# Performance work log

Measured on AMD Instinct MI355X. Metric: run time of the kernel, lower is better.

## Reference

```python
import jax, jax.numpy as jnp
import numpy as np

NUM_HEADS = 16
NUM_HIDDENS = 1024
NEG_INF = -1e6


def setup_inputs() -> dict:
    key = jax.random.key(0)
    ks = jax.random.split(key, 8)
    B, S, D = 2, 2048, NUM_HIDDENS
    scale = 1.0 / np.sqrt(D)
    return {
        "q": jax.random.normal(ks[0], (B, S, D), jnp.float32),
        "k": jax.random.normal(ks[1], (B, S, D), jnp.float32),
        "v": jax.random.normal(ks[2], (B, S, D), jnp.float32),
        # nn.Linear weights have shape (out_features, in_features)
        "Wq": jax.random.normal(ks[3], (D, D), jnp.float32) * scale,
        "Wk": jax.random.normal(ks[4], (D, D), jnp.float32) * scale,
        "Wv": jax.random.normal(ks[5], (D, D), jnp.float32) * scale,
        "Wo": jax.random.normal(ks[6], (D, D), jnp.float32) * scale,
        "valid_len": jax.random.randint(ks[7], (B,), 1, 2048 + 1, jnp.int32),
    }


def _unpack_heads(x, nh):
    # (B, S, H) -> (B*nh, S, H//nh), matching Unpack_base_head
    B, S, H = x.shape
    return x.reshape(B, S, nh, H // nh).transpose(0, 2, 1, 3).reshape(B * nh, S, H // nh)


def _merge_heads(x, nh):
    # Faithful to Merge_base_head: (B*nh, S, dh) -> (B, nh, S, dh)
    # -> permute(0,2,3,1) -> (B, S, dh, nh) -> (B, S, dh*nh)
    Bnh, S, dh = x.shape
    B = Bnh // nh
    x = x.reshape(B, nh, S, dh).transpose(0, 2, 3, 1)
    return x.reshape(B, S, dh * nh)


def reference(q, k, v, Wq, Wk, Wv, Wo, valid_len):
    nh = NUM_HEADS
    # projections (bias=False); Linear: x @ W.T
    qh = _unpack_heads(q @ Wq.T, nh)  # (B*nh, S, dh)
    kh = _unpack_heads(k @ Wk.T, nh)
    vh = _unpack_heads(v @ Wv.T, nh)
    dh = qh.shape[-1]
    scores = jnp.einsum("bqd,bkd->bqk", qh, kh) / jnp.sqrt(jnp.float32(dh))
    # repeat_interleave valid_len by num_heads along dim 0
    vl = jnp.repeat(valid_len, nh)  # (B*nh,)
    key_pos = jnp.arange(scores.shape[-1])  # (S,)
    mask = key_pos[None, None, :] < vl[:, None, None]  # (B*nh, 1, S)
    scores = jnp.where(mask, scores, NEG_INF)
    attn = jax.nn.softmax(scores, axis=-1)  # dropout=0.0 (eval) -> identity
    out = jnp.einsum("bqk,bkd->bqd", attn, vh)  # (B*nh, S, dh)
    out = _merge_heads(out, nh) @ Wo.T  # (B, S, H)
    return out, attn
```

## Files before the change

kernel.cpp:

```cpp
#include <hip/hip_runtime.h>
#include <stdint.h>

#define SB 2048
#define DB 1024
#define NHB 16
#define DHB 64

typedef __attribute__((ext_vector_type(8))) short short8;
typedef __attribute__((ext_vector_type(4))) short short4v;
typedef __attribute__((ext_vector_type(4))) float f32x4;

#define SC2 0.18033688011112042f

__device__ __forceinline__ unsigned short f2bf(float f) {
  union { float f; uint32_t u; } v; v.f = f;
  uint32_t u = v.u;
  return (unsigned short)((u + 0x7FFFu + ((u >> 16) & 1u)) >> 16);
}

__device__ __forceinline__ void gld16(const void* g, void* l) {
  __builtin_amdgcn_global_load_lds(
      (const __attribute__((address_space(1))) void*)g,
      (__attribute__((address_space(3))) void*)l, 16, 0, 0);
}

__device__ __forceinline__ int xcd_swz(int bid, int nwg) {
  return (bid & 7) * (nwg >> 3) + (bid >> 3);
}

struct ConvArgs {
  const float* s[6];
  unsigned short* d[6];
  int n[6];
};

__global__ __launch_bounds__(256) void conv_kernel(ConvArgs a) {
  const int t = blockIdx.y;
  const float* __restrict__ src = a.s[t];
  unsigned short* __restrict__ dst = a.d[t];
  const int n8 = a.n[t] >> 3;
  for (int i = blockIdx.x * 256 + threadIdx.x; i < n8; i += gridDim.x * 256) {
    const f32x4* p = (const f32x4*)src + (size_t)i * 2;
    f32x4 x = p[0], y = p[1];
    short8 o;
    o[0] = (short)f2bf(x[0]); o[1] = (short)f2bf(x[1]);
    o[2] = (short)f2bf(x[2]); o[3] = (short)f2bf(x[3]);
    o[4] = (short)f2bf(y[0]); o[5] = (short)f2bf(y[1]);
    o[6] = (short)f2bf(y[2]); o[7] = (short)f2bf(y[3]);
    *(short8*)(dst + (size_t)i * 8) = o;
  }
}

__global__ __launch_bounds__(256) void woperm_kernel(
    const float* __restrict__ Wo, unsigned short* __restrict__ Wob) {
  for (int i = blockIdx.x * 256 + threadIdx.x; i < DB * DB; i += gridDim.x * 256) {
    int o = i >> 10, cp = i & 1023;
    int src = (o << 10) + ((cp & 63) << 4) + (cp >> 6);
    Wob[i] = f2bf(Wo[src]);
  }
}

struct GemmArgs {
  const unsigned short* A[3];
  const unsigned short* B[3];
  void* O[3];
  int mode[3];
};

__global__ __launch_bounds__(256) void gemm128(GemmArgs ga) {
  __shared__ unsigned short SH[17408];
  unsigned short* Ab = SH;
  unsigned short* Bb = SH + 8192;

  const int z = blockIdx.y;
  const unsigned short* __restrict__ A = ga.A[z];
  const unsigned short* __restrict__ Bw = ga.B[z];
  const int mode = ga.mode[z];

  const int tid = threadIdx.x;
  const int w = tid >> 6, lane = tid & 63;
  const int g = lane >> 4, li = lane & 15;
  const int wm = w >> 1, wn = w & 1;
  const int l = xcd_swz(blockIdx.x, 256);
  const int m0 = (l >> 3) * 128, n0 = (l & 7) * 128;

  const int srow = lane >> 3;
  const int sg = (lane & 7) ^ srow;

  f32x4 acc[4][4];
  #pragma unroll
  for (int i = 0; i < 4; ++i)
    #pragma unroll
    for (int j = 0; j < 4; ++j)
      #pragma unroll
      for (int e = 0; e < 4; ++e) acc[i][j][e] = 0.f;

  for (int k0 = 0; k0 < DB; k0 += 64) {
    __syncthreads();
    #pragma unroll
    for (int i = 0; i < 4; ++i) {
      int c = w * 4 + i;
      gld16(A + (size_t)(m0 + c * 8 + srow) * DB + k0 + sg * 8, Ab + c * 512);
      gld16(Bw + (size_t)(n0 + c * 8 + srow) * DB + k0 + sg * 8, Bb + c * 512);
    }
    __syncthreads();
    short8 af[4][2], bf[4][2];
    #pragma unroll
    for (int mf = 0; mf < 4; ++mf)
      #pragma unroll
      for (int ks = 0; ks < 2; ++ks)
        af[mf][ks] = *(const short8*)&Ab[(wm * 64 + mf * 16 + li) * 64 +
                                         (((ks * 4 + g) ^ (li & 7)) << 3)];
    #pragma unroll
    for (int nf = 0; nf < 4; ++nf)
      #pragma unroll
      for (int ks = 0; ks < 2; ++ks)
        bf[nf][ks] = *(const short8*)&Bb[(wn * 64 + nf * 16 + li) * 64 +
                                         (((ks * 4 + g) ^ (li & 7)) << 3)];
    __builtin_amdgcn_s_setprio(1);
    #pragma unroll
    for (int ks = 0; ks < 2; ++ks)
      #pragma unroll
      for (int mf = 0; mf < 4; ++mf)
        #pragma unroll
        for (int nf = 0; nf < 4; ++nf)
          acc[mf][nf] = __builtin_amdgcn_mfma_f32_16x16x32_bf16(
              af[mf][ks], bf[nf][ks], acc[mf][nf], 0, 0, 0);
    __builtin_amdgcn_s_setprio(0);
  }

  if (mode == 0) {
    unsigned short* O = (unsigned short*)ga.O[z];
    #pragma unroll
    for (int mf = 0; mf < 4; ++mf)
      #pragma unroll
      for (int nf = 0; nf < 4; ++nf)
        #pragma unroll
        for (int r = 0; r < 4; ++r) {
          int row = m0 + wm * 64 + mf * 16 + g * 4 + r;
          int col = n0 + wn * 64 + nf * 16 + li;
          int b_ = row >> 11, s_ = row & 2047;
          int h = col >> 6, dp = col & 63;
          O[((size_t)(b_ * NHB + h) * SB + s_) * DHB + dp] = f2bf(acc[mf][nf][r]);
        }
  } else {
    unsigned short* O = (unsigned short*)ga.O[z];
    __syncthreads();
    #pragma unroll
    for (int mf = 0; mf < 4; ++mf)
      #pragma unroll
      for (int nf = 0; nf < 4; ++nf) {
        short4v pk;
        #pragma unroll
        for (int r = 0; r < 4; ++r) pk[r] = (short)f2bf(acc[mf][nf][r]);
        *(short4v*)&SH[(size_t)(wn * 64 + nf * 16 + li) * 136 +
                       wm * 64 + mf * 16 + g * 4] = pk;
      }
    __syncthreads();
    int c = tid >> 1, rh = tid & 1;
    int col = n0 + c;
    int h = col >> 6, dp = col & 63;
    int b_ = m0 >> 11, s0 = (m0 & 2047) + rh * 64;
    unsigned short* dst = O + ((size_t)(b_ * NHB + h) * DHB + dp) * SB + s0;
    #pragma unroll
    for (int j = 0; j < 8; ++j)
      *(short8*)(dst + j * 8) = *(const short8*)&SH[c * 136 + rh * 64 + j * 8];
  }
}

__global__ __launch_bounds__(256) void attn_kernel(
    const unsigned short* __restrict__ Qh, const unsigned short* __restrict__ Kh,
    const unsigned short* __restrict__ Vt, const int* __restrict__ valid_len,
    float* __restrict__ attn_out, unsigned short* __restrict__ Mg)
{
  __shared__ unsigned short Kb[2][4096];
  __shared__ unsigned short Vb[2][4096];
  __shared__ unsigned short P[64][72];

  const int tid = threadIdx.x;
  const int wave = tid >> 6, lane = tid & 63;
  const int g = lane >> 4, li = lane & 15;
  const int lsw = xcd_swz(blockIdx.x, 1024);
  const int xcd = lsw >> 7, j = lsw & 127;
  const int bh = ((j >> 6) << 4) + xcd * 2 + ((j >> 5) & 1);
  const int q0 = (j & 31) * 64;
  const int b_ = bh >> 4;
  const int vl = valid_len[b_];
  const int nkt = min(32, (vl + 63) >> 6);

  const int srow = lane >> 3;
  const int sg = (lane & 7) ^ srow;

  const size_t kbase = (size_t)bh * SB * DHB;
  const size_t vbase = (size_t)bh * DHB * SB;

  const int qrow_l = q0 + wave * 16 + li;
  short8 qa[2];
  qa[0] = *(const short8*)(Qh + ((size_t)bh * SB + qrow_l) * DHB + g * 8);
  qa[1] = *(const short8*)(Qh + ((size_t)bh * SB + qrow_l) * DHB + 32 + g * 8);

  float lQ = 0.f;

  {
    const int c = wave * 2;
    gld16(Kh + kbase + (size_t)(c * 8 + srow) * DHB + sg * 8, &Kb[0][c * 512]);
    gld16(Kh + kbase + (size_t)((c + 1) * 8 + srow) * DHB + sg * 8,
          &Kb[0][(c + 1) * 512]);
    int cur = 0;
    for (int kti = 0; kti < nkt; ++kti) {
      __syncthreads();
      if (kti + 1 < nkt) {
        int kn = (kti + 1) * 64;
        gld16(Kh + kbase + (size_t)(kn + c * 8 + srow) * DHB + sg * 8,
              &Kb[cur ^ 1][c * 512]);
        gld16(Kh + kbase + (size_t)(kn + (c + 1) * 8 + srow) * DHB + sg * 8,
              &Kb[cur ^ 1][(c + 1) * 512]);
      }
      const int kt = kti * 64;
      f32x4 sc[4];
      #pragma unroll
      for (int nf = 0; nf < 4; ++nf)
        #pragma unroll
        for (int e = 0; e < 4; ++e) sc[nf][e] = 0.f;
      __builtin_amdgcn_s_setprio(1);
      #pragma unroll
      for (int ks = 0; ks < 2; ++ks)
        #pragma unroll
        for (int nf = 0; nf < 4; ++nf) {
          short8 kbf = *(const short8*)&Kb[cur][(nf * 16 + li) * 64 +
                                               (((ks * 4 + g) ^ (li & 7)) << 3)];
          sc[nf] = __builtin_amdgcn_mfma_f32_16x16x32_bf16(kbf, qa[ks], sc[nf], 0, 0, 0);
        }
      __builtin_amdgcn_s_setprio(0);
      float la = 0.f;
      #pragma unroll
      for (int nf = 0; nf < 4; ++nf)
        #pragma unroll
        for (int r = 0; r < 4; ++r) {
          int key = kt + nf * 16 + g * 4 + r;
          float s2 = (key < vl) ? sc[nf][r] * SC2 : -1.5e6f;
          la += exp2f(s2);
        }
      lQ += la;
      cur ^= 1;
    }
  }
  __syncthreads();

  float L = lQ;
  L += __shfl_xor(L, 16);
  L += __shfl_xor(L, 32);
  const float rlQ = 1.f / L;

  f32x4 oacc[4];
  #pragma unroll
  for (int nf = 0; nf < 4; ++nf)
    #pragma unroll
    for (int e = 0; e < 4; ++e) oacc[nf][e] = 0.f;

  {
    const int c = wave * 2;
    gld16(Kh + kbase + (size_t)(c * 8 + srow) * DHB + sg * 8, &Kb[0][c * 512]);
    gld16(Kh + kbase + (size_t)((c + 1) * 8 + srow) * DHB + sg * 8,
          &Kb[0][(c + 1) * 512]);
    gld16(Vt + vbase + (size_t)(c * 8 + srow) * SB + sg * 8, &Vb[0][c * 512]);
    gld16(Vt + vbase + (size_t)((c + 1) * 8 + srow) * SB + sg * 8,
          &Vb[0][(c + 1) * 512]);
    int cur = 0;
    for (int kti = 0; kti < nkt; ++kti) {
      __syncthreads();
      if (kti + 1 < nkt) {
        int kn = (kti + 1) * 64;
        gld16(Kh + kbase + (size_t)(kn + c * 8 + srow) * DHB + sg * 8,
              &Kb[cur ^ 1][c * 512]);
        gld16(Kh + kbase + (size_t)(kn + (c + 1) * 8 + srow) * DHB + sg * 8,
              &Kb[cur ^ 1][(c + 1) * 512]);
        gld16(Vt + vbase + (size_t)(c * 8 + srow) * SB + kn + sg * 8,
              &Vb[cur ^ 1][c * 512]);
        gld16(Vt + vbase + (size_t)((c + 1) * 8 + srow) * SB + kn + sg * 8,
              &Vb[cur ^ 1][(c + 1) * 512]);
      }
      const int kt = kti * 64;
      f32x4 sc[4];
      #pragma unroll
      for (int nf = 0; nf < 4; ++nf)
        #pragma unroll
        for (int e = 0; e < 4; ++e) sc[nf][e] = 0.f;
      __builtin_amdgcn_s_setprio(1);
      #pragma unroll
      for (int ks = 0; ks < 2; ++ks)
        #pragma unroll
        for (int nf = 0; nf < 4; ++nf) {
          short8 kbf = *(const short8*)&Kb[cur][(nf * 16 + li) * 64 +
                                               (((ks * 4 + g) ^ (li & 7)) << 3)];
          sc[nf] = __builtin_amdgcn_mfma_f32_16x16x32_bf16(kbf, qa[ks], sc[nf], 0, 0, 0);
        }
      __builtin_amdgcn_s_setprio(0);
      #pragma unroll
      for (int nf = 0; nf < 4; ++nf) {
        short4v pk;
        #pragma unroll
        for (int r = 0; r < 4; ++r) {
          int key = kt + nf * 16 + g * 4 + r;
          float s2 = (key < vl) ? sc[nf][r] * SC2 : -1.5e6f;
          float p = exp2f(s2) * rlQ;
          sc[nf][r] = p;
          pk[r] = (short)f2bf(p);
        }
        __builtin_nontemporal_store(
            sc[nf],
            (f32x4*)(attn_out + (size_t)bh * SB * SB + (size_t)qrow_l * SB +
                     kt + nf * 16 + g * 4));
        *(short4v*)&P[wave * 16 + li][nf * 16 + g * 4] = pk;
      }
      __builtin_amdgcn_s_setprio(1);
      #pragma unroll
      for (int ks = 0; ks < 2; ++ks) {
        short8 pa = *(const short8*)&P[wave * 16 + li][ks * 32 + g * 8];
        #pragma unroll
        for (int nf = 0; nf < 4; ++nf) {
          short8 vbf = *(const short8*)&Vb[cur][(nf * 16 + li) * 64 +
                                               (((ks * 4 + g) ^ (li & 7)) << 3)];
          oacc[nf] = __builtin_amdgcn_mfma_f32_16x16x32_bf16(pa, vbf, oacc[nf], 0, 0, 0);
        }
      }
      __builtin_amdgcn_s_setprio(0);
      cur ^= 1;
    }
  }

  {
    int c0 = nkt * 64;
    int rem4 = (SB - c0) >> 2;
    if (rem4 > 0) {
      f32x4 z;
      z[0] = 0.f; z[1] = 0.f; z[2] = 0.f; z[3] = 0.f;
      for (int row = 0; row < 64; ++row) {
        float* dst = attn_out + (size_t)bh * SB * SB + (size_t)(q0 + row) * SB + c0;
        for (int c = tid; c < rem4; c += 256)
          __builtin_nontemporal_store(z, (f32x4*)dst + c);
      }
    }
  }

  __syncthreads();
  const int h = bh & 15;
  #pragma unroll
  for (int nf = 0; nf < 4; ++nf) {
    short4v ok;
    #pragma unroll
    for (int r = 0; r < 4; ++r) ok[r] = (short)f2bf(oacc[nf][r]);
    #pragma unroll
    for (int r = 0; r < 4; ++r)
      P[wave * 16 + g * 4 + r][nf * 16 + li] = (unsigned short)ok[r];
  }
  __syncthreads();
  {
    int row = tid >> 2, seg = tid & 3;
    unsigned short* dst = Mg + ((size_t)b_ * SB + q0 + row) * DB + h * 64 + seg * 16;
    *(short8*)dst       = *(const short8*)&P[row][seg * 16];
    *(short8*)(dst + 8) = *(const short8*)&P[row][seg * 16 + 8];
  }
}

__global__ __launch_bounds__(256) void outproj_kernel(
    const unsigned short* __restrict__ A, const unsigned short* __restrict__ Bw,
    float* __restrict__ Out)
{
  __shared__ unsigned short SH[12288];
  unsigned short* Ab = SH;
  unsigned short* Bb = SH + 8192;

  const int tid = threadIdx.x;
  const int w = tid >> 6, lane = tid & 63;
  const int g = lane >> 4, li = lane & 15;
  const int wm = w >> 1, wn = w & 1;
  const int l = xcd_swz(blockIdx.x, 512);
  const int m0 = (l >> 4) * 128, n0 = (l & 15) * 64;

  const int srow = lane >> 3;
  const int sg = (lane & 7) ^ srow;

  int a_off[4][2], b_off[2][2];
  #pragma unroll
  for (int mf = 0; mf < 4; ++mf) {
    int row = wm * 64 + mf * 16 + li;
    #pragma unroll
    for (int ks = 0; ks < 2; ++ks)
      a_off[mf][ks] = row * 64 + (((ks * 4 + g) ^ (li & 7)) << 3);
  }
  #pragma unroll
  for (int nf = 0; nf < 2; ++nf) {
    int row = wn * 32 + nf * 16 + li;
    #pragma unroll
    for (int ks = 0; ks < 2; ++ks)
      b_off[nf][ks] = row * 64 + (((ks * 4 + g) ^ (li & 7)) << 3);
  }

  f32x4 acc[4][2];
  #pragma unroll
  for (int i = 0; i < 4; ++i)
    #pragma unroll
    for (int j = 0; j < 2; ++j)
      #pragma unroll
      for (int e = 0; e < 4; ++e) acc[i][j][e] = 0.f;

  for (int k0 = 0; k0 < DB; k0 += 64) {
    __syncthreads();
    #pragma unroll
    for (int i = 0; i < 4; ++i) {
      int c = w * 4 + i;
      gld16(A + (size_t)(m0 + c * 8 + srow) * DB + k0 + sg * 8, Ab + c * 512);
    }
    #pragma unroll
    for (int i = 0; i < 2; ++i) {
      int c = w * 2 + i;
      gld16(Bw + (size_t)(n0 + c * 8 + srow) * DB + k0 + sg * 8, Bb + c * 512);
    }
    __syncthreads();
    short8 af[4][2], bf[2][2];
    #pragma unroll
    for (int mf = 0; mf < 4; ++mf)
      #pragma unroll
      for (int ks = 0; ks < 2; ++ks)
        af[mf][ks] = *(const short8*)&Ab[a_off[mf][ks]];
    #pragma unroll
    for (int nf = 0; nf < 2; ++nf)
      #pragma unroll
      for (int ks = 0; ks < 2; ++ks)
        bf[nf][ks] = *(const short8*)&Bb[b_off[nf][ks]];
    __builtin_amdgcn_s_setprio(1);
    #pragma unroll
    for (int ks = 0; ks < 2; ++ks)
      #pragma unroll
      for (int mf = 0; mf < 4; ++mf)
        #pragma unroll
        for (int nf = 0; nf < 2; ++nf)
          acc[mf][nf] = __builtin_amdgcn_mfma_f32_16x16x32_bf16(
              af[mf][ks], bf[nf][ks], acc[mf][nf], 0, 0, 0);
    __builtin_amdgcn_s_setprio(0);
  }

  #pragma unroll
  for (int mf = 0; mf < 4; ++mf)
    #pragma unroll
    for (int nf = 0; nf < 2; ++nf)
      #pragma unroll
      for (int r = 0; r < 4; ++r) {
        int row = m0 + wm * 64 + mf * 16 + g * 4 + r;
        int col = n0 + wn * 32 + nf * 16 + li;
        Out[(size_t)row * DB + col] = acc[mf][nf][r];
      }
}

extern "C" void kernel_launch(void* const* d_in, const int* in_sizes, int n_in,
                              void* d_out, int out_size, void* d_ws, size_t ws_size,
                              hipStream_t stream) {
  const float* q  = (const float*)d_in[0];
  const float* k  = (const float*)d_in[1];
  const float* v  = (const float*)d_in[2];
  const float* Wq = (const float*)d_in[3];
  const float* Wk = (const float*)d_in[4];
  const float* Wv = (const float*)d_in[5];
  const float* Wo = (const float*)d_in[6];
  const int* vlen = (const int*)d_in[7];

  const size_t HS = (size_t)2 * NHB * SB * DHB;
  const size_t WS = (size_t)DB * DB;

  unsigned short* ws = (unsigned short*)d_ws;
  unsigned short* qb  = ws;
  unsigned short* kb  = qb + HS;
  unsigned short* vb  = kb + HS;
  unsigned short* Wqb = vb + HS;
  unsigned short* Wkb = Wqb + WS;
  unsigned short* Wvb = Wkb + WS;
  unsigned short* Wob = Wvb + WS;
  unsigned short* Qh  = Wob + WS;
  unsigned short* Kh  = Qh + HS;
  unsigned short* Vt  = Kh + HS;
  unsigned short* Mg  = qb;

  float* out  = (float*)d_out;
  float* attn = out + (size_t)2 * SB * DB;

  ConvArgs ca;
  ca.s[0] = q;  ca.d[0] = qb;  ca.n[0] = (int)HS;
  ca.s[1] = k;  ca.d[1] = kb;  ca.n[1] = (int)HS;
  ca.s[2] = v;  ca.d[2] = vb;  ca.n[2] = (int)HS;
  ca.s[3] = Wq; ca.d[3] = Wqb; ca.n[3] = (int)WS;
  ca.s[4] = Wk; ca.d[4] = Wkb; ca.n[4] = (int)WS;
  ca.s[5] = Wv; ca.d[5] = Wvb; ca.n[5] = (int)WS;

  GemmArgs pa;
  pa.A[0] = qb;  pa.A[1] = kb;  pa.A[2] = vb;
  pa.B[0] = Wqb; pa.B[1] = Wkb; pa.B[2] = Wvb;
  pa.O[0] = Qh;  pa.O[1] = Kh;  pa.O[2] = Vt;
  pa.mode[0] = 0; pa.mode[1] = 0; pa.mode[2] = 1;

  dim3 blk(256);
  conv_kernel<<<dim3(1024, 6), blk, 0, stream>>>(ca);
  woperm_kernel<<<dim3(512), blk, 0, stream>>>(Wo, Wob);
  gemm128<<<dim3(256, 3), blk, 0, stream>>>(pa);
  attn_kernel<<<dim3(1024), blk, 0, stream>>>(Qh, Kh, Vt, vlen, attn, Mg);
  outproj_kernel<<<dim3(512), blk, 0, stream>>>(Mg, Wob, out);
}
```

Measured before the change: 224.1 us.

## Split attention into row-sum pass and output pass; fold Wo conversion into conv

```diff
diff --git a/kernel.cpp b/kernel.cpp
--- a/kernel.cpp
+++ b/kernel.cpp
@@ -34,8 +34,18 @@
   int n[6];
 };
 
-__global__ __launch_bounds__(256) void conv_kernel(ConvArgs a) {
+__global__ __launch_bounds__(256) void conv_kernel(ConvArgs a,
+                                                   const float* __restrict__ Wo,
+                                                   unsigned short* __restrict__ Wob) {
   const int t = blockIdx.y;
+  if (t == 6) {
+    for (int i = blockIdx.x * 256 + threadIdx.x; i < DB * DB; i += gridDim.x * 256) {
+      int o = i >> 10, cp = i & 1023;
+      int src = (o << 10) + ((cp & 63) << 4) + (cp >> 6);
+      Wob[i] = f2bf(Wo[src]);
+    }
+    return;
+  }
   const float* __restrict__ src = a.s[t];
   unsigned short* __restrict__ dst = a.d[t];
   const int n8 = a.n[t] >> 3;
@@ -51,15 +61,6 @@
   }
 }
 
-__global__ __launch_bounds__(256) void woperm_kernel(
-    const float* __restrict__ Wo, unsigned short* __restrict__ Wob) {
-  for (int i = blockIdx.x * 256 + threadIdx.x; i < DB * DB; i += gridDim.x * 256) {
-    int o = i >> 10, cp = i & 1023;
-    int src = (o << 10) + ((cp & 63) << 4) + (cp >> 6);
-    Wob[i] = f2bf(Wo[src]);
-  }
-}
-
 struct GemmArgs {
   const unsigned short* A[3];
   const unsigned short* B[3];
@@ -168,38 +169,37 @@
   }
 }
 
-__global__ __launch_bounds__(256) void attn_kernel(
+__global__ __launch_bounds__(256) void lsum_kernel(
     const unsigned short* __restrict__ Qh, const unsigned short* __restrict__ Kh,
-    const unsigned short* __restrict__ Vt, const int* __restrict__ valid_len,
-    float* __restrict__ attn_out, unsigned short* __restrict__ Mg)
+    const int* __restrict__ valid_len, float* __restrict__ RL)
 {
   __shared__ unsigned short Kb[2][4096];
-  __shared__ unsigned short Vb[2][4096];
-  __shared__ unsigned short P[64][72];
 
   const int tid = threadIdx.x;
   const int wave = tid >> 6, lane = tid & 63;
   const int g = lane >> 4, li = lane & 15;
-  const int lsw = xcd_swz(blockIdx.x, 1024);
-  const int xcd = lsw >> 7, j = lsw & 127;
-  const int bh = ((j >> 6) << 4) + xcd * 2 + ((j >> 5) & 1);
-  const int q0 = (j & 31) * 64;
+  const int lsw = xcd_swz(blockIdx.x, 512);
+  const int xcd = lsw >> 6, j = lsw & 63;
+  const int bh = ((j >> 5) << 4) + xcd * 2 + ((j >> 4) & 1);
+  const int q0 = (j & 15) * 128;
   const int b_ = bh >> 4;
   const int vl = valid_len[b_];
   const int nkt = min(32, (vl + 63) >> 6);
 
   const int srow = lane >> 3;
   const int sg = (lane & 7) ^ srow;
-
   const size_t kbase = (size_t)bh * SB * DHB;
-  const size_t vbase = (size_t)bh * DHB * SB;
-
-  const int qrow_l = q0 + wave * 16 + li;
-  short8 qa[2];
-  qa[0] = *(const short8*)(Qh + ((size_t)bh * SB + qrow_l) * DHB + g * 8);
-  qa[1] = *(const short8*)(Qh + ((size_t)bh * SB + qrow_l) * DHB + 32 + g * 8);
-
-  float lQ = 0.f;
+
+  short8 qa[2][2];
+  #pragma unroll
+  for (int qf = 0; qf < 2; ++qf)
+    #pragma unroll
+    for (int ks = 0; ks < 2; ++ks)
+      qa[qf][ks] = *(const short8*)(
+          Qh + ((size_t)bh * SB + q0 + wave * 32 + qf * 16 + li) * DHB +
+          ks * 32 + g * 8);
+
+  float lQ[2] = {0.f, 0.f};
 
   {
     const int c = wave * 2;
@@ -217,11 +217,13 @@
               &Kb[cur ^ 1][(c + 1) * 512]);
       }
       const int kt = kti * 64;
-      f32x4 sc[4];
-      #pragma unroll
-      for (int nf = 0; nf < 4; ++nf)
-        #pragma unroll
-        for (int e = 0; e < 4; ++e) sc[nf][e] = 0.f;
+      f32x4 sc[2][4];
+      #pragma unroll
+      for (int qf = 0; qf < 2; ++qf)
+        #pragma unroll
+        for (int nf = 0; nf < 4; ++nf)
+          #pragma unroll
+          for (int e = 0; e < 4; ++e) sc[qf][nf][e] = 0.f;
       __builtin_amdgcn_s_setprio(1);
       #pragma unroll
       for (int ks = 0; ks < 2; ++ks)
@@ -229,28 +231,83 @@
         for (int nf = 0; nf < 4; ++nf) {
           short8 kbf = *(const short8*)&Kb[cur][(nf * 16 + li) * 64 +
                                                (((ks * 4 + g) ^ (li & 7)) << 3)];
-          sc[nf] = __builtin_amdgcn_mfma_f32_16x16x32_bf16(kbf, qa[ks], sc[nf], 0, 0, 0);
+          #pragma unroll
+          for (int qf = 0; qf < 2; ++qf)
+            sc[qf][nf] = __builtin_amdgcn_mfma_f32_16x16x32_bf16(
+                kbf, qa[qf][ks], sc[qf][nf], 0, 0, 0);
         }
       __builtin_amdgcn_s_setprio(0);
-      float la = 0.f;
-      #pragma unroll
-      for (int nf = 0; nf < 4; ++nf)
-        #pragma unroll
-        for (int r = 0; r < 4; ++r) {
-          int key = kt + nf * 16 + g * 4 + r;
-          float s2 = (key < vl) ? sc[nf][r] * SC2 : -1.5e6f;
-          la += exp2f(s2);
-        }
-      lQ += la;
+      if (kt + 64 <= vl) {
+        #pragma unroll
+        for (int qf = 0; qf < 2; ++qf) {
+          float la = 0.f;
+          #pragma unroll
+          for (int nf = 0; nf < 4; ++nf)
+            #pragma unroll
+            for (int r = 0; r < 4; ++r) la += exp2f(sc[qf][nf][r] * SC2);
+          lQ[qf] += la;
+        }
+      } else {
+        #pragma unroll
+        for (int qf = 0; qf < 2; ++qf) {
+          float la = 0.f;
+          #pragma unroll
+          for (int nf = 0; nf < 4; ++nf)
+            #pragma unroll
+            for (int r = 0; r < 4; ++r) {
+              int key = kt + nf * 16 + g * 4 + r;
+              float s2 = (key < vl) ? sc[qf][nf][r] * SC2 : -1.5e6f;
+              la += exp2f(s2);
+            }
+          lQ[qf] += la;
+        }
+      }
       cur ^= 1;
     }
   }
-  __syncthreads();
-
-  float L = lQ;
-  L += __shfl_xor(L, 16);
-  L += __shfl_xor(L, 32);
-  const float rlQ = 1.f / L;
+
+  #pragma unroll
+  for (int qf = 0; qf < 2; ++qf) {
+    float L = lQ[qf];
+    L += __shfl_xor(L, 16);
+    L += __shfl_xor(L, 32);
+    if (lane < 16)
+      RL[(size_t)bh * SB + q0 + wave * 32 + qf * 16 + li] = 1.f / L;
+  }
+}
+
+__global__ __launch_bounds__(256) void attn2_kernel(
+    const unsigned short* __restrict__ Qh, const unsigned short* __restrict__ Kh,
+    const unsigned short* __restrict__ Vt, const int* __restrict__ valid_len,
+    const float* __restrict__ RL, float* __restrict__ attn_out,
+    unsigned short* __restrict__ Mg)
+{
+  __shared__ unsigned short Kb[2][4096];
+  __shared__ unsigned short Vb[2][4096];
+  __shared__ unsigned short P[64][72];
+
+  const int tid = threadIdx.x;
+  const int wave = tid >> 6, lane = tid & 63;
+  const int g = lane >> 4, li = lane & 15;
+  const int lsw = xcd_swz(blockIdx.x, 1024);
+  const int xcd = lsw >> 7, j = lsw & 127;
+  const int bh = ((j >> 6) << 4) + xcd * 2 + ((j >> 5) & 1);
+  const int q0 = (j & 31) * 64;
+  const int b_ = bh >> 4;
+  const int vl = valid_len[b_];
+  const int nkt = min(32, (vl + 63) >> 6);
+
+  const int srow = lane >> 3;
+  const int sg = (lane & 7) ^ srow;
+
+  const size_t kbase = (size_t)bh * SB * DHB;
+  const size_t vbase = (size_t)bh * DHB * SB;
+
+  const int qrow_l = q0 + wave * 16 + li;
+  short8 qa[2];
+  qa[0] = *(const short8*)(Qh + ((size_t)bh * SB + qrow_l) * DHB + g * 8);
+  qa[1] = *(const short8*)(Qh + ((size_t)bh * SB + qrow_l) * DHB + 32 + g * 8);
+  const float rlQ = RL[(size_t)bh * SB + qrow_l];
 
   f32x4 oacc[4];
   #pragma unroll
@@ -296,16 +353,26 @@
           sc[nf] = __builtin_amdgcn_mfma_f32_16x16x32_bf16(kbf, qa[ks], sc[nf], 0, 0, 0);
         }
       __builtin_amdgcn_s_setprio(0);
+      const bool fullt = (kt + 64 <= vl);
       #pragma unroll
       for (int nf = 0; nf < 4; ++nf) {
         short4v pk;
-        #pragma unroll
-        for (int r = 0; r < 4; ++r) {
-          int key = kt + nf * 16 + g * 4 + r;
-          float s2 = (key < vl) ? sc[nf][r] * SC2 : -1.5e6f;
-          float p = exp2f(s2) * rlQ;
-          sc[nf][r] = p;
-          pk[r] = (short)f2bf(p);
+        if (fullt) {
+          #pragma unroll
+          for (int r = 0; r < 4; ++r) {
+            float p = exp2f(sc[nf][r] * SC2) * rlQ;
+            sc[nf][r] = p;
+            pk[r] = (short)f2bf(p);
+          }
+        } else {
+          #pragma unroll
+          for (int r = 0; r < 4; ++r) {
+            int key = kt + nf * 16 + g * 4 + r;
+            float s2 = (key < vl) ? sc[nf][r] * SC2 : -1.5e6f;
+            float p = exp2f(s2) * rlQ;
+            sc[nf][r] = p;
+            pk[r] = (short)f2bf(p);
+          }
         }
         __builtin_nontemporal_store(
             sc[nf],
@@ -346,14 +413,10 @@
   __syncthreads();
   const int h = bh & 15;
   #pragma unroll
-  for (int nf = 0; nf < 4; ++nf) {
-    short4v ok;
-    #pragma unroll
-    for (int r = 0; r < 4; ++r) ok[r] = (short)f2bf(oacc[nf][r]);
+  for (int nf = 0; nf < 4; ++nf)
     #pragma unroll
     for (int r = 0; r < 4; ++r)
-      P[wave * 16 + g * 4 + r][nf * 16 + li] = (unsigned short)ok[r];
-  }
+      P[wave * 16 + g * 4 + r][nf * 16 + li] = f2bf(oacc[nf][r]);
   __syncthreads();
   {
     int row = tid >> 2, seg = tid & 3;
@@ -479,6 +542,7 @@
   unsigned short* Qh  = Wob + WS;
   unsigned short* Kh  = Qh + HS;
   unsigned short* Vt  = Kh + HS;
+  float* RL           = (float*)(Vt + HS);
   unsigned short* Mg  = qb;
 
   float* out  = (float*)d_out;
@@ -499,9 +563,9 @@
   pa.mode[0] = 0; pa.mode[1] = 0; pa.mode[2] = 1;
 
   dim3 blk(256);
-  conv_kernel<<<dim3(1024, 6), blk, 0, stream>>>(ca);
-  woperm_kernel<<<dim3(512), blk, 0, stream>>>(Wo, Wob);
+  conv_kernel<<<dim3(1024, 7), blk, 0, stream>>>(ca, Wo, Wob);
   gemm128<<<dim3(256, 3), blk, 0, stream>>>(pa);
-  attn_kernel<<<dim3(1024), blk, 0, stream>>>(Qh, Kh, Vt, vlen, attn, Mg);
+  lsum_kernel<<<dim3(512), blk, 0, stream>>>(Qh, Kh, vlen, RL);
+  attn2_kernel<<<dim3(1024), blk, 0, stream>>>(Qh, Kh, Vt, vlen, RL, attn, Mg);
   outproj_kernel<<<dim3(512), blk, 0, stream>>>(Mg, Wob, out);
 }
```

New measurement: 249.3 us. 11.2% more time.
